# Performance work log

Hardware: AMD Instinct MI355X
Metric: run time of the kernel (lower is better)

## Reference

```python
import jax, jax.numpy as jnp
import numpy as np

B, M, N, D, J, C = 2, 384, 96, 512, 640, 1024


def setup_inputs() -> dict:
    key = jax.random.key(0)
    ks = jax.random.split(key, 8)
    s = lambda k, shape, fan: jax.random.normal(k, shape, dtype=jnp.float32) / np.sqrt(fan)
    return {
        "encoder_out": jax.random.normal(ks[0], (B, M, D), dtype=jnp.float32),
        "decoder_out": jax.random.normal(ks[1], (B, N, D), dtype=jnp.float32),
        "w_audio": s(ks[2], (D, J), D),
        "b_audio": jnp.zeros((J,), dtype=jnp.float32),
        "w_text": s(ks[3], (D, J), D),
        "b_text": jnp.zeros((J,), dtype=jnp.float32),
        "w_join": s(ks[4], (J, C), J),
        "b_join": jnp.zeros((C,), dtype=jnp.float32),
    }


def reference(encoder_out, decoder_out, w_audio, b_audio, w_text, b_text, w_join, b_join):
    # audio_fc / text_fc projections to joint space
    a = jnp.einsum("bmd,dj->bmj", encoder_out, w_audio) + b_audio  # [B,M,J]
    t = jnp.einsum("bnd,dj->bnj", decoder_out, w_text) + b_text    # [B,N,J]
    # _join: broadcast add over (M,N), tanh, then join_net linear to vocab
    h = jnp.tanh(a[:, :, None, :] + t[:, None, :, :])              # [B,M,N,J]
    logits = jnp.einsum("bmnj,jc->bmnc", h, w_join) + b_join       # [B,M,N,C]
    return logits
```

## Files before the change

### kernel.cpp

```cpp
#include <hip/hip_runtime.h>
#include <hip/hip_bf16.h>


typedef float f32x4 __attribute__((ext_vector_type(4)));
typedef short short8 __attribute__((ext_vector_type(8)));

__device__ float g_A[768 * 640];
__device__ float g_T[192 * 640];
__device__ short g_W2[80 * 1024 * 8];

__device__ __forceinline__ unsigned short f2bf(float f) {
    unsigned u = __float_as_uint(f);
    unsigned r = u + 0x7fffu + ((u >> 16) & 1u);
    return (unsigned short)(r >> 16);
}

__device__ __forceinline__ float fast_tanh(float x) {
    x = fminf(fmaxf(x, -10.f), 10.f);
    float e2 = __expf(x * 2.0f);
    return 1.f - 2.f / (e2 + 1.f);
}

__global__ __launch_bounds__(320) void prep_kernel(
    const float* __restrict__ enc, const float* __restrict__ dec,
    const float* __restrict__ w_audio, const float* __restrict__ b_audio,
    const float* __restrict__ w_text,  const float* __restrict__ b_text,
    const float* __restrict__ w_join)
{
    const int bid = blockIdx.x, tid = threadIdx.x;
    if (bid < 240) {
        const float *X, *W, *bias; float* O; int row0;
        if (bid < 192) { X = enc; W = w_audio; bias = b_audio; O = g_A; row0 = bid * 4; }
        else           { X = dec; W = w_text;  bias = b_text;  O = g_T; row0 = (bid - 192) * 4; }
        __shared__ float xs[4][512];
        for (int i = tid; i < 4 * 128; i += 320) {
            int r = i >> 7, q = i & 127;
            ((f32x4*)xs[r])[q] = ((const f32x4*)(X + (size_t)(row0 + r) * 512))[q];
        }
        __syncthreads();
        float acc[4][2] = {};
        const int j0 = tid * 2;
        const float2* Wp = (const float2*)W;
        #pragma unroll 4
        for (int k = 0; k < 512; ++k) {
            float2 wv = Wp[k * 320 + tid];
            #pragma unroll
            for (int r = 0; r < 4; ++r) {
                acc[r][0] = fmaf(xs[r][k], wv.x, acc[r][0]);
                acc[r][1] = fmaf(xs[r][k], wv.y, acc[r][1]);
            }
        }
        float2 bv = *(const float2*)(bias + j0);
        #pragma unroll
        for (int r = 0; r < 4; ++r) {
            float2 o = make_float2(acc[r][0] + bv.x, acc[r][1] + bv.y);
            *(float2*)(O + (row0 + r) * 640 + j0) = o;
        }
    } else {
        int idx = (bid - 240) * 320 + tid;
        int g = idx >> 10, c = idx & 1023;
        short8 v;
        #pragma unroll
        for (int j = 0; j < 8; ++j)
            v[j] = (short)f2bf(w_join[(g * 8 + j) * 1024 + c]);
        ((short8*)g_W2)[idx] = v;
    }
}

__global__ __launch_bounds__(256, 2) void join_kernel(
    const float* __restrict__ b_join,
    float* __restrict__ out)
{
    __shared__ char hb[64 * 1280];
    const int tid = threadIdx.x;
    const int r0  = blockIdx.x * 64;

    for (int e = tid; e < 64 * 160; e += 256) {
        int row = e / 160;
        int q   = e - row * 160;
        int r   = r0 + row;
        int arow = r / 96;
        int trow = (r / 36864) * 96 + (r - arow * 96);
        int j = q * 4;
        f32x4 av = *(const f32x4*)(g_A + arow * 640 + j);
        f32x4 tv = *(const f32x4*)(g_T + trow * 640 + j);
        float h0 = fast_tanh(av[0] + tv[0]);
        float h1 = fast_tanh(av[1] + tv[1]);
        float h2 = fast_tanh(av[2] + tv[2]);
        float h3 = fast_tanh(av[3] + tv[3]);
        unsigned lo = (unsigned)f2bf(h0) | ((unsigned)f2bf(h1) << 16);
        unsigned hi = (unsigned)f2bf(h2) | ((unsigned)f2bf(h3) << 16);
        unsigned off = row * 1280 + (((unsigned)((q >> 1) ^ (row & 7))) << 4) + (q & 1) * 8;
        *(uint2*)(hb + off) = make_uint2(lo, hi);
    }
    __syncthreads();

    const int lane = tid & 63;
    const int wave = tid >> 6;
    const int l15  = lane & 15;
    const int quad = lane >> 4;

    for (int ct = 0; ct < 4; ++ct) {
        const int colw = ct * 256 + wave * 64;
        f32x4 acc[4][4] = {};
        for (int kb = 0; kb < 640; kb += 32) {
            const int g = (kb >> 3) + quad;
            short8 af[4], bf[4];
            #pragma unroll
            for (int mt = 0; mt < 4; ++mt) {
                int row = mt * 16 + l15;
                af[mt] = *(const short8*)(hb + row * 1280 + ((unsigned)(g ^ (row & 7)) << 4));
            }
            #pragma unroll
            for (int nt = 0; nt < 4; ++nt) {
                int col = colw + nt * 16 + l15;
                bf[nt] = *(const short8*)(g_W2 + ((size_t)g * 1024 + col) * 8);
            }
            #pragma unroll
            for (int mt = 0; mt < 4; ++mt)
                #pragma unroll
                for (int nt = 0; nt < 4; ++nt)
                    acc[mt][nt] = __builtin_amdgcn_mfma_f32_16x16x32_bf16(
                        bf[nt], af[mt], acc[mt][nt], 0, 0, 0);
        }
        f32x4 bj[4];
        #pragma unroll
        for (int nt = 0; nt < 4; ++nt)
            bj[nt] = *(const f32x4*)(b_join + colw + nt * 16 + quad * 4);
        #pragma unroll
        for (int mt = 0; mt < 4; ++mt) {
            float* orow = out + (size_t)(r0 + mt * 16 + l15) * 1024;
            #pragma unroll
            for (int nt = 0; nt < 4; ++nt) {
                int c4 = colw + nt * 16 + quad * 4;
                f32x4 v = acc[mt][nt] + bj[nt];
                __builtin_nontemporal_store(v, (f32x4*)(orow + c4));
            }
        }
    }
}

extern "C" void kernel_launch(void* const* d_in, const int* in_sizes, int n_in,
                              void* d_out, int out_size, void* d_ws, size_t ws_size,
                              hipStream_t stream) {
    const float* enc     = (const float*)d_in[0];
    const float* dec     = (const float*)d_in[1];
    const float* w_audio = (const float*)d_in[2];
    const float* b_audio = (const float*)d_in[3];
    const float* w_text  = (const float*)d_in[4];
    const float* b_text  = (const float*)d_in[5];
    const float* w_join  = (const float*)d_in[6];
    const float* b_join  = (const float*)d_in[7];
    float* out = (float*)d_out;

    prep_kernel<<<dim3(496), dim3(320), 0, stream>>>(
        enc, dec, w_audio, b_audio, w_text, b_text, w_join);
    join_kernel<<<dim3(1152), dim3(256), 0, stream>>>(b_join, out);
}
```

Measured before the change: 502.1 us.

## Move projections to split-bf16 MFMA, halve join tile and double-buffer fragments

The fp32 scalar projection GEMMs are replaced by a pack kernel plus a proj kernel. The pack kernel splits inputs and weights into bf16 hi/lo pairs, and the proj kernel computes the products with three bf16 MFMAs per tile to approximate fp32 accuracy. The join kernel now uses 32-row tiles with occupancy 4 instead of 64 rows with occupancy 2, and software-pipelines the A/B fragment loads across k-steps. This adds a third launch and extra packed buffers, and the proj kernel runs on only 30 blocks, so that stage is poorly parallelised.

```diff
diff --git a/kernel.cpp b/kernel.cpp
--- a/kernel.cpp
+++ b/kernel.cpp
@@ -8,74 +8,135 @@
 __device__ float g_A[768 * 640];
 __device__ float g_T[192 * 640];
 __device__ short g_W2[80 * 1024 * 8];
+__device__ short g_Xph[960 * 512];
+__device__ short g_Xpl[960 * 512];
+__device__ short g_Wph[2 * 64 * 640 * 8];
+__device__ short g_Wpl[2 * 64 * 640 * 8];
 
 __device__ __forceinline__ unsigned short f2bf(float f) {
     unsigned u = __float_as_uint(f);
     unsigned r = u + 0x7fffu + ((u >> 16) & 1u);
     return (unsigned short)(r >> 16);
 }
-
+__device__ __forceinline__ float bf2f(unsigned short h) {
+    return __uint_as_float((unsigned)h << 16);
+}
 __device__ __forceinline__ float fast_tanh(float x) {
     x = fminf(fmaxf(x, -10.f), 10.f);
     float e2 = __expf(x * 2.0f);
     return 1.f - 2.f / (e2 + 1.f);
 }
 
-__global__ __launch_bounds__(320) void prep_kernel(
+__global__ __launch_bounds__(256) void pack_kernel(
     const float* __restrict__ enc, const float* __restrict__ dec,
-    const float* __restrict__ w_audio, const float* __restrict__ b_audio,
-    const float* __restrict__ w_text,  const float* __restrict__ b_text,
+    const float* __restrict__ w_audio, const float* __restrict__ w_text,
     const float* __restrict__ w_join)
 {
-    const int bid = blockIdx.x, tid = threadIdx.x;
-    if (bid < 240) {
-        const float *X, *W, *bias; float* O; int row0;
-        if (bid < 192) { X = enc; W = w_audio; bias = b_audio; O = g_A; row0 = bid * 4; }
-        else           { X = dec; W = w_text;  bias = b_text;  O = g_T; row0 = (bid - 192) * 4; }
-        __shared__ float xs[4][512];
-        for (int i = tid; i < 4 * 128; i += 320) {
-            int r = i >> 7, q = i & 127;
-            ((f32x4*)xs[r])[q] = ((const f32x4*)(X + (size_t)(row0 + r) * 512))[q];
-        }
-        __syncthreads();
-        float acc[4][2] = {};
-        const int j0 = tid * 2;
-        const float2* Wp = (const float2*)W;
-        #pragma unroll 4
-        for (int k = 0; k < 512; ++k) {
-            float2 wv = Wp[k * 320 + tid];
-            #pragma unroll
-            for (int r = 0; r < 4; ++r) {
-                acc[r][0] = fmaf(xs[r][k], wv.x, acc[r][0]);
-                acc[r][1] = fmaf(xs[r][k], wv.y, acc[r][1]);
+    int idx = blockIdx.x * 256 + threadIdx.x;
+    if (idx < 61440) {
+        int row = idx >> 6, g = idx & 63;
+        const float* src = (row < 768) ? (enc + (size_t)row * 512)
+                                       : (dec + (size_t)(row - 768) * 512);
+        short8 hi, lo;
+        #pragma unroll
+        for (int i = 0; i < 8; ++i) {
+            float x = src[g * 8 + i];
+            unsigned short h = f2bf(x);
+            hi[i] = (short)h;
+            lo[i] = (short)f2bf(x - bf2f(h));
+        }
+        size_t off = ((size_t)(row >> 4) * 64 + g) * 16 + (row & 15);
+        ((short8*)g_Xph)[off] = hi;
+        ((short8*)g_Xpl)[off] = lo;
+    } else if (idx < 143360) {
+        int e = idx - 61440;
+        int mat = e / 40960; e -= mat * 40960;
+        int g = e / 640, j = e - g * 640;
+        const float* W = mat ? w_text : w_audio;
+        short8 hi, lo;
+        #pragma unroll
+        for (int i = 0; i < 8; ++i) {
+            float x = W[(size_t)(g * 8 + i) * 640 + j];
+            unsigned short h = f2bf(x);
+            hi[i] = (short)h;
+            lo[i] = (short)f2bf(x - bf2f(h));
+        }
+        size_t off = (size_t)(mat * 64 + g) * 640 + j;
+        ((short8*)g_Wph)[off] = hi;
+        ((short8*)g_Wpl)[off] = lo;
+    } else {
+        int e = idx - 143360;
+        int g = e >> 10, c = e & 1023;
+        short8 v;
+        #pragma unroll
+        for (int j = 0; j < 8; ++j)
+            v[j] = (short)f2bf(w_join[(size_t)(g * 8 + j) * 1024 + c]);
+        ((short8*)g_W2)[e] = v;
+    }
+}
+
+__global__ __launch_bounds__(256) void proj_kernel(
+    const float* __restrict__ b_audio, const float* __restrict__ b_text)
+{
+    const int bid = blockIdx.x;
+    const int mtile = bid >> 1, nhalf = bid & 1;
+    const int tid  = threadIdx.x;
+    const int lane = tid & 63, wave = tid >> 6, l15 = lane & 15, quad = lane >> 4;
+    const int mat  = (mtile >= 12) ? 1 : 0;
+    const int colw = nhalf * 320 + wave * 80;
+    const float* bias = mat ? b_text : b_audio;
+    float* O = mat ? g_T : g_A;
+    const int orow0 = mtile * 64 - mat * 768;
+
+    const short8* Xh = (const short8*)g_Xph;
+    const short8* Xl = (const short8*)g_Xpl;
+    const short8* Wh = (const short8*)g_Wph;
+    const short8* Wl = (const short8*)g_Wpl;
+
+    f32x4 acc[4][5] = {};
+    for (int kb = 0; kb < 512; kb += 32) {
+        const int g = (kb >> 3) + quad;
+        short8 ah[4], al[4], bh[5], bl[5];
+        #pragma unroll
+        for (int mt = 0; mt < 4; ++mt) {
+            size_t xo = ((size_t)(mtile * 4 + mt) * 64 + g) * 16 + l15;
+            ah[mt] = Xh[xo]; al[mt] = Xl[xo];
+        }
+        #pragma unroll
+        for (int nt = 0; nt < 5; ++nt) {
+            size_t wo = (size_t)(mat * 64 + g) * 640 + colw + nt * 16 + l15;
+            bh[nt] = Wh[wo]; bl[nt] = Wl[wo];
+        }
+        #pragma unroll
+        for (int mt = 0; mt < 4; ++mt)
+            #pragma unroll
+            for (int nt = 0; nt < 5; ++nt) {
+                acc[mt][nt] = __builtin_amdgcn_mfma_f32_16x16x32_bf16(bh[nt], ah[mt], acc[mt][nt], 0, 0, 0);
+                acc[mt][nt] = __builtin_amdgcn_mfma_f32_16x16x32_bf16(bh[nt], al[mt], acc[mt][nt], 0, 0, 0);
+                acc[mt][nt] = __builtin_amdgcn_mfma_f32_16x16x32_bf16(bl[nt], ah[mt], acc[mt][nt], 0, 0, 0);
             }
-        }
-        float2 bv = *(const float2*)(bias + j0);
-        #pragma unroll
-        for (int r = 0; r < 4; ++r) {
-            float2 o = make_float2(acc[r][0] + bv.x, acc[r][1] + bv.y);
-            *(float2*)(O + (row0 + r) * 640 + j0) = o;
-        }
-    } else {
-        int idx = (bid - 240) * 320 + tid;
-        int g = idx >> 10, c = idx & 1023;
-        short8 v;
-        #pragma unroll
-        for (int j = 0; j < 8; ++j)
-            v[j] = (short)f2bf(w_join[(g * 8 + j) * 1024 + c]);
-        ((short8*)g_W2)[idx] = v;
-    }
-}
-
-__global__ __launch_bounds__(256, 2) void join_kernel(
+    }
+    #pragma unroll
+    for (int nt = 0; nt < 5; ++nt) {
+        const int c4 = colw + nt * 16 + quad * 4;
+        f32x4 bj = *(const f32x4*)(bias + c4);
+        #pragma unroll
+        for (int mt = 0; mt < 4; ++mt) {
+            f32x4 v = acc[mt][nt] + bj;
+            *(f32x4*)(O + (size_t)(orow0 + mt * 16 + l15) * 640 + c4) = v;
+        }
+    }
+}
+
+__global__ __launch_bounds__(256, 4) void join_kernel(
     const float* __restrict__ b_join,
     float* __restrict__ out)
 {
-    __shared__ char hb[64 * 1280];
+    __shared__ char hb[32 * 1280];
     const int tid = threadIdx.x;
-    const int r0  = blockIdx.x * 64;
-
-    for (int e = tid; e < 64 * 160; e += 256) {
+    const int r0  = blockIdx.x * 32;
+
+    for (int e = tid; e < 32 * 160; e += 256) {
         int row = e / 160;
         int q   = e - row * 160;
         int r   = r0 + row;
@@ -100,35 +161,51 @@
     const int l15  = lane & 15;
     const int quad = lane >> 4;
 
+    auto ldaf = [&](short8* af, int g) {
+        #pragma unroll
+        for (int mt = 0; mt < 2; ++mt) {
+            int rw = mt * 16 + l15;
+            af[mt] = *(const short8*)(hb + rw * 1280 + ((unsigned)(g ^ (rw & 7)) << 4));
+        }
+    };
+    auto ldbf = [&](short8* bf, int g, int colw) {
+        #pragma unroll
+        for (int nt = 0; nt < 4; ++nt)
+            bf[nt] = *(const short8*)(g_W2 + ((size_t)g * 1024 + colw + nt * 16 + l15) * 8);
+    };
+
     for (int ct = 0; ct < 4; ++ct) {
         const int colw = ct * 256 + wave * 64;
-        f32x4 acc[4][4] = {};
-        for (int kb = 0; kb < 640; kb += 32) {
-            const int g = (kb >> 3) + quad;
-            short8 af[4], bf[4];
-            #pragma unroll
-            for (int mt = 0; mt < 4; ++mt) {
-                int row = mt * 16 + l15;
-                af[mt] = *(const short8*)(hb + row * 1280 + ((unsigned)(g ^ (row & 7)) << 4));
-            }
-            #pragma unroll
-            for (int nt = 0; nt < 4; ++nt) {
-                int col = colw + nt * 16 + l15;
-                bf[nt] = *(const short8*)(g_W2 + ((size_t)g * 1024 + col) * 8);
-            }
-            #pragma unroll
-            for (int mt = 0; mt < 4; ++mt)
+        f32x4 acc[2][4] = {};
+        short8 afA[2], bfA[4], afB[2], bfB[4];
+        ldaf(afA, quad); ldbf(bfA, quad, colw);
+        #pragma unroll
+        for (int kb = 0; kb < 640; kb += 64) {
+            const int gB = (kb >> 3) + 4 + quad;
+            ldaf(afB, gB); ldbf(bfB, gB, colw);
+            #pragma unroll
+            for (int mt = 0; mt < 2; ++mt)
                 #pragma unroll
                 for (int nt = 0; nt < 4; ++nt)
                     acc[mt][nt] = __builtin_amdgcn_mfma_f32_16x16x32_bf16(
-                        bf[nt], af[mt], acc[mt][nt], 0, 0, 0);
+                        bfA[nt], afA[mt], acc[mt][nt], 0, 0, 0);
+            if (kb + 64 < 640) {
+                const int gA2 = (kb >> 3) + 8 + quad;
+                ldaf(afA, gA2); ldbf(bfA, gA2, colw);
+            }
+            #pragma unroll
+            for (int mt = 0; mt < 2; ++mt)
+                #pragma unroll
+                for (int nt = 0; nt < 4; ++nt)
+                    acc[mt][nt] = __builtin_amdgcn_mfma_f32_16x16x32_bf16(
+                        bfB[nt], afB[mt], acc[mt][nt], 0, 0, 0);
         }
         f32x4 bj[4];
         #pragma unroll
         for (int nt = 0; nt < 4; ++nt)
             bj[nt] = *(const f32x4*)(b_join + colw + nt * 16 + quad * 4);
         #pragma unroll
-        for (int mt = 0; mt < 4; ++mt) {
+        for (int mt = 0; mt < 2; ++mt) {
             float* orow = out + (size_t)(r0 + mt * 16 + l15) * 1024;
             #pragma unroll
             for (int nt = 0; nt < 4; ++nt) {
@@ -153,7 +230,7 @@
     const float* b_join  = (const float*)d_in[7];
     float* out = (float*)d_out;
 
-    prep_kernel<<<dim3(496), dim3(320), 0, stream>>>(
-        enc, dec, w_audio, b_audio, w_text, b_text, w_join);
-    join_kernel<<<dim3(1152), dim3(256), 0, stream>>>(b_join, out);
-}
+    pack_kernel<<<dim3(880), dim3(256), 0, stream>>>(enc, dec, w_audio, w_text, w_join);
+    proj_kernel<<<dim3(30), dim3(256), 0, stream>>>(b_audio, b_text);
+    join_kernel<<<dim3(2304), dim3(256), 0, stream>>>(b_join, out);
+}
```

New measurement: 764.4 us. 52.3% more time.
